# Kernel tuning notes

Hardware: AMD Instinct MI355X
Metric: run time of the kernel (lower is better)

Reference implementation:

```python
import jax, jax.numpy as jnp
import numpy as np

B, L, DP, DS = 8, 256, 128, 256  # batch, length, d_pair, d_seq (= 2*d_pair)
NEAR = 4
K = 3  # k_base=3 (no trbv emb); full mask + 2 chains => every row valid


def _ln(x, g, b):
    mu = x.mean(-1, keepdims=True)
    var = ((x - mu) ** 2).mean(-1, keepdims=True)
    return (x - mu) / jnp.sqrt(var + 1e-5) * g + b


def _masked_mean(x, m, axes):
    num = (x * m).sum(axes)
    den = jnp.clip(m.sum(axes), 1e-6, None)
    return num / den


def _masked_max(x, m, axes):
    v = jnp.where(m > 0, x, -jnp.inf).max(axes)
    return jnp.where(jnp.isinf(v), jnp.zeros_like(v), v)


def _mlp(x, w1, b1, w2, b2):
    return jax.nn.relu(x @ w1 + b1) @ w2 + b2


def setup_inputs() -> dict:
    key = jax.random.key(0)
    ks = jax.random.split(key, 26)
    s = 0.02
    d = {
        "seq_repr": jax.random.normal(ks[0], (B, L, DS), jnp.float32),
        "pair_repr": jax.random.normal(ks[1], (B, L, L, DP), jnp.float32),
        "chain_id": jax.random.randint(ks[2], (B, L), 0, 2, jnp.int32),
        "mask": jnp.ones((B, L), jnp.bool_),
        "ln_s_g": jnp.ones((DS,), jnp.float32),
        "ln_s_b": jnp.zeros((DS,), jnp.float32),
        "ln_z_g": jnp.ones((DS,), jnp.float32),
        "ln_z_b": jnp.zeros((DS,), jnp.float32),
        "W_seq": jax.random.normal(ks[3], (DS, DS), jnp.float32) * s,
        "W_pair": jax.random.normal(ks[4], (DS, DS), jnp.float32) * s,
    }
    in_dim = 2 * DS
    for i, name in enumerate(["m0", "m1", "m2"]):
        d[name + "_w1"] = jax.random.normal(ks[5 + 4 * i], (in_dim, 64), jnp.float32) * s
        d[name + "_b1"] = jnp.zeros((64,), jnp.float32)
        d[name + "_w2"] = jax.random.normal(ks[6 + 4 * i], (64, 1), jnp.float32) * s
        d[name + "_b2"] = jnp.zeros((1,), jnp.float32)
    d["f_w1"] = jax.random.normal(ks[20], (3, 8), jnp.float32) * s
    d["f_b1"] = jnp.zeros((8,), jnp.float32)
    d["f_w2"] = jax.random.normal(ks[21], (8, 1), jnp.float32) * s
    d["f_b2"] = jnp.zeros((1,), jnp.float32)
    return d


def reference(seq_repr, pair_repr, chain_id, mask,
              ln_s_g, ln_s_b, ln_z_g, ln_z_b, W_seq, W_pair,
              m0_w1, m0_b1, m0_w2, m0_b2,
              m1_w1, m1_b1, m1_w2, m1_b2,
              m2_w1, m2_b1, m2_w2, m2_b2,
              f_w1, f_b1, f_w2, f_b2):
    m = mask.astype(jnp.float32)[..., None]  # [B,L,1]
    s = _ln(seq_repr, ln_s_g, ln_s_b) @ W_seq  # [B,L,DS]
    s_mean = _masked_mean(s, m, 1)
    s_max = _masked_max(s, m, 1)
    s_feat = jnp.concatenate([s_mean, s_max], -1)  # [B,2*DS]

    pair = jnp.concatenate([pair_repr, jnp.swapaxes(pair_repr, 1, 2)], -1)  # [B,L,L,DS]
    eye = jnp.eye(L, dtype=pair.dtype)[None, :, :, None]
    pair = pair * (1.0 - eye)
    z = _ln(pair, ln_z_g, ln_z_b) @ W_pair  # [B,L,L,DS]

    pm = (mask[:, :, None] & mask[:, None, :]).astype(jnp.float32)[..., None]  # [B,L,L,1]
    same = (chain_id[:, :, None] == chain_id[:, None, :])[..., None]
    intra = pm * same.astype(jnp.float32)
    inter = pm * (~same).astype(jnp.float32)

    inter_mean = _masked_mean(z, inter, (1, 2))  # [B,DS]
    row_den_raw = inter.sum(2)  # [B,L,1]
    row_valid = row_den_raw[..., 0] > 0
    row_mean_i = (z * inter).sum(2) / jnp.clip(row_den_raw, 1e-6, None)  # [B,L,DS]
    score = jnp.where(row_valid, jnp.linalg.norm(row_mean_i, axis=-1), -1e9)
    _, topk_idx = jax.lax.top_k(score, K)  # [B,K]
    selected = jnp.take_along_axis(row_mean_i, topk_idx[..., None], axis=1)
    inter_peak = selected.mean(1)
    inter_feat = jnp.concatenate([inter_mean, inter_peak], -1)

    idx = jnp.arange(L)
    diff = jnp.abs(idx[:, None] - idx[None, :])
    band = ((diff <= NEAR) & (diff > 0)).astype(jnp.float32)[None, :, :, None]
    intra_near = intra * band
    intra_compact = _masked_mean(z, intra_near, (1, 2))
    intra_max = _masked_max(z, intra_near, (1, 2))
    intra_feat = jnp.concatenate([intra_compact, intra_max], -1)

    logits = jnp.concatenate([
        _mlp(s_feat, m0_w1, m0_b1, m0_w2, m0_b2),
        _mlp(inter_feat, m1_w1, m1_b1, m1_w2, m1_b2),
        _mlp(intra_feat, m2_w1, m2_b1, m2_w2, m2_b2),
    ], axis=1)  # [B,3]
    return jax.nn.relu(logits @ f_w1 + f_b1) @ f_w2 + f_b2  # [B,1]
```

## Files before the change

kernel.cpp:

```cpp
#include <hip/hip_runtime.h>
#include <math.h>

#define NB 8
#define NL 256
#define NDP 128
#define NDS 256
#define NEARB 4


__device__ __forceinline__ float waveSum(float v) {
#pragma unroll
  for (int m = 1; m < 64; m <<= 1) v += __shfl_xor(v, m);
  return v;
}

__device__ __forceinline__ void waveSum2(float& a, float& b) {
#pragma unroll
  for (int m = 1; m < 64; m <<= 1) {
    a += __shfl_xor(a, m);
    b += __shfl_xor(b, m);
  }
}

__device__ __forceinline__ void grpSum2(float& a, float& b) {
#pragma unroll
  for (int m = 1; m < 32; m <<= 1) {
    a += __shfl_xor(a, m);
    b += __shfl_xor(b, m);
  }
}

__global__ __launch_bounds__(256) void kA_pair(
    const float* __restrict__ pair, const int* __restrict__ chain,
    const float* __restrict__ g, const float* __restrict__ beta,
    const float* __restrict__ Wp, const float* __restrict__ seq,
    const float* __restrict__ gs, const float* __restrict__ bs,
    const float* __restrict__ Ws, float* __restrict__ acc,
    float* __restrict__ cntI, float* __restrict__ sbuf,
    float* __restrict__ intraLN, float* __restrict__ cntA,
    float* __restrict__ bandMax) {
  const int i = blockIdx.x;
  const int b = blockIdx.y;
  const int tid = threadIdx.x;
  const int wave = tid >> 6, lane = tid & 63;
  const int grp = lane >> 5, pos = lane & 31;
  const int slot = wave * 2 + grp;

  __shared__ int sList[NL];
  __shared__ int sCnt4[4];
  __shared__ int sOff[4];
  __shared__ int sN;
  __shared__ float sAcc[8][NDS];
  __shared__ float sU[8];
  __shared__ float lnrow[8][NDS];
  __shared__ float red[4], red2[4];

  const int ci = chain[b * NL + i];

  {
    float v = seq[(size_t)(b * NL + i) * NDS + tid];
    float s = v, ssq = v * v;
    waveSum2(s, ssq);
    if (lane == 0) {
      red[wave] = s;
      red2[wave] = ssq;
    }
    __syncthreads();
    float S = red[0] + red[1] + red[2] + red[3];
    float SS = red2[0] + red2[1] + red2[2] + red2[3];
    float mu = S * (1.0f / NDS);
    float inv = 1.0f / sqrtf(SS * (1.0f / NDS) - mu * mu + 1e-5f);
    lnrow[0][tid] = (v - mu) * inv * gs[tid] + bs[tid];
    __syncthreads();
    float z = 0.f;
    for (int k = 0; k < NDS; ++k) z = fmaf(lnrow[0][k], Ws[k * NDS + tid], z);
    sbuf[(size_t)(b * NL + i) * NDS + tid] = z;
  }
  __syncthreads();

  {
    const bool flag = (chain[b * NL + tid] != ci);
    unsigned long long bal = __ballot(flag);
    int ppos = __popcll(bal & ((1ull << lane) - 1ull));
    if (lane == 0) sCnt4[wave] = __popcll(bal);
    __syncthreads();
    if (tid == 0) {
      int o = 0;
#pragma unroll
      for (int w = 0; w < 4; ++w) {
        sOff[w] = o;
        o += sCnt4[w];
      }
      sN = o;
    }
    __syncthreads();
    if (flag) sList[sOff[wave] + ppos] = tid;
    __syncthreads();

    const int n = sN;
    const int c0 = 8 * pos;

    const bool rowHalf = (pos < 16);
    const float* sb = rowHalf ? pair + ((size_t)(b * NL + i) * NL) * NDP + c0
                              : pair + ((size_t)b * NL * NL) * NDP +
                                    (size_t)i * NDP + (c0 - NDP);
    const size_t jstr = rowHalf ? (size_t)NDP : (size_t)NL * NDP;

    float R0 = 0.f, R1 = 0.f, R2 = 0.f, R3 = 0.f;
    float R4 = 0.f, R5 = 0.f, R6 = 0.f, R7 = 0.f;
    float U = 0.f;

    for (int p = slot; p < n; p += 8) {
      const int j = sList[p];
      const float* src = sb + (size_t)j * jstr;
      float4 a0 = *(const float4*)src;
      float4 a1 = *(const float4*)(src + 4);
      float s = (a0.x + a0.y) + (a0.z + a0.w) + (a1.x + a1.y) + (a1.z + a1.w);
      float ss = a0.x * a0.x + a0.y * a0.y + a0.z * a0.z + a0.w * a0.w +
                 a1.x * a1.x + a1.y * a1.y + a1.z * a1.z + a1.w * a1.w;
      grpSum2(s, ss);
      const float mu = s * (1.0f / NDS);
      const float inv = 1.0f / sqrtf(ss * (1.0f / NDS) - mu * mu + 1e-5f);
      R0 = fmaf(a0.x, inv, R0);
      R1 = fmaf(a0.y, inv, R1);
      R2 = fmaf(a0.z, inv, R2);
      R3 = fmaf(a0.w, inv, R3);
      R4 = fmaf(a1.x, inv, R4);
      R5 = fmaf(a1.y, inv, R5);
      R6 = fmaf(a1.z, inv, R6);
      R7 = fmaf(a1.w, inv, R7);
      U = fmaf(mu, inv, U);
    }

    *(float4*)&sAcc[slot][c0] = make_float4(R0, R1, R2, R3);
    *(float4*)&sAcc[slot][c0 + 4] = make_float4(R4, R5, R6, R7);
    sU[slot] = U;
    __syncthreads();
    float v = 0.f;
#pragma unroll
    for (int p2 = 0; p2 < 8; ++p2) v += sAcc[p2][tid];
    float Utot = sU[0] + sU[1] + sU[2] + sU[3] + sU[4] + sU[5] + sU[6] + sU[7];
    acc[(size_t)(b * NL + i) * NDS + tid] =
        g[tid] * (v - Utot) + (float)n * beta[tid];
    if (tid == 0) cntI[b * NL + i] = (float)n;
  }

  {
    const int t = tid;
    int js[8];
    int nv = 0;
    for (int dj = -NEARB; dj <= NEARB; ++dj) {
      int j = i + dj;
      if (dj == 0 || j < 0 || j >= NL) continue;
      if (chain[b * NL + j] == ci) js[nv++] = j;
    }

    const int c0 = 4 * lane;
    const float4 g4 = *(const float4*)(g + c0);
    const float4 b4 = *(const float4*)(beta + c0);
    __syncthreads();
    for (int r = wave; r < 8; r += 4) {
      if (r < nv) {
        const int j = js[r];
        const float* src =
            (lane < 32)
                ? pair + ((size_t)(b * NL + i) * NL + j) * NDP + c0
                : pair + ((size_t)(b * NL + j) * NL + i) * NDP + (c0 - NDP);
        float4 a = *(const float4*)src;
        float s = (a.x + a.y) + (a.z + a.w);
        float ss = a.x * a.x + a.y * a.y + a.z * a.z + a.w * a.w;
        waveSum2(s, ss);
        float mu = s * (1.0f / NDS);
        float inv = 1.0f / sqrtf(ss * (1.0f / NDS) - mu * mu + 1e-5f);
        lnrow[r][c0] = (a.x - mu) * inv * g4.x + b4.x;
        lnrow[r][c0 + 1] = (a.y - mu) * inv * g4.y + b4.y;
        lnrow[r][c0 + 2] = (a.z - mu) * inv * g4.z + b4.z;
        lnrow[r][c0 + 3] = (a.w - mu) * inv * g4.w + b4.w;
      } else {
        lnrow[r][c0] = 0.f;
        lnrow[r][c0 + 1] = 0.f;
        lnrow[r][c0 + 2] = 0.f;
        lnrow[r][c0 + 3] = 0.f;
      }
    }
    __syncthreads();

    float z[8] = {0, 0, 0, 0, 0, 0, 0, 0};
    if (nv > 0) {
      for (int k = 0; k < NDS; ++k) {
        float wk = Wp[k * NDS + t];
#pragma unroll
        for (int r = 0; r < 8; ++r) z[r] += lnrow[r][k] * wk;
      }
    }
    float zmax = -INFINITY, lnsum = 0.f;
#pragma unroll
    for (int r = 0; r < 8; ++r)
      if (r < nv) {
        zmax = fmaxf(zmax, z[r]);
        lnsum += lnrow[r][t];
      }
    intraLN[(size_t)(b * NL + i) * NDS + t] = lnsum;
    bandMax[(size_t)(b * NL + i) * NDS + t] = zmax;
    if (t == 0) cntA[b * NL + i] = (float)nv;
  }
}

__global__ __launch_bounds__(256) void kB_rowmean(
    const float* __restrict__ acc, const float* __restrict__ cntI,
    const float* __restrict__ Wp, const float* __restrict__ sbuf,
    const float* __restrict__ intraLN, const float* __restrict__ cntA,
    const float* __restrict__ bandMax, float* __restrict__ rmean,
    float* __restrict__ score, float* __restrict__ part,
    float* __restrict__ partC) {
  const int chunk = blockIdx.x;
  const int b = blockIdx.y;
  const int t = threadIdx.x;
  const int wave = t >> 6, lane = t & 63;
  __shared__ float vrow[4][NDS];
  __shared__ float red[4];
  float cnts[4], araw[4];
#pragma unroll
  for (int r = 0; r < 4; ++r) {
    const int i = chunk * 4 + r;
    float c = cntI[b * NL + i];
    cnts[r] = c;
    araw[r] = acc[(size_t)(b * NL + i) * NDS + t];
    vrow[r][t] = araw[r] / fmaxf(c, 1e-6f);
  }
  __syncthreads();
  float z[4] = {0, 0, 0, 0};
  for (int k = 0; k < NDS; ++k) {
    float wk = Wp[k * NDS + t];
#pragma unroll
    for (int r = 0; r < 4; ++r) z[r] += vrow[r][k] * wk;
  }
#pragma unroll
  for (int r = 0; r < 4; ++r) {
    const int i = chunk * 4 + r;
    rmean[(size_t)(b * NL + i) * NDS + t] = z[r];
    float q = waveSum(z[r] * z[r]);
    __syncthreads();
    if (lane == 0) red[wave] = q;
    __syncthreads();
    if (t == 0) {
      float ss = red[0] + red[1] + red[2] + red[3];
      score[b * NL + i] = (cnts[r] > 0.f) ? sqrtf(ss) : -1e9f;
    }
    __syncthreads();
  }

  float ssum = 0.f, smax = -INFINITY, isum = 0.f, imax = -INFINITY;
  const float asum = araw[0] + araw[1] + araw[2] + araw[3];
#pragma unroll
  for (int r = 0; r < 4; ++r) {
    const size_t idx = (size_t)(b * NL + chunk * 4 + r) * NDS + t;
    float v = sbuf[idx];
    ssum += v;
    smax = fmaxf(smax, v);
    isum += intraLN[idx];
    imax = fmaxf(imax, bandMax[idx]);
  }
  const size_t pb = (size_t)(b * 64 + chunk) * 5 * NDS;
  part[pb + 0 * NDS + t] = ssum;
  part[pb + 1 * NDS + t] = smax;
  part[pb + 2 * NDS + t] = asum;
  part[pb + 3 * NDS + t] = isum;
  part[pb + 4 * NDS + t] = imax;
  if (t == 0) {
    partC[(b * 64 + chunk) * 2 + 0] = cnts[0] + cnts[1] + cnts[2] + cnts[3];
    float ia = 0.f;
    for (int r = 0; r < 4; ++r) ia += cntA[b * NL + chunk * 4 + r];
    partC[(b * 64 + chunk) * 2 + 1] = ia;
  }
}

__global__ __launch_bounds__(256) void kC_heads(
    const float* __restrict__ part, const float* __restrict__ partC,
    const float* __restrict__ Wp, const float* __restrict__ score,
    const float* __restrict__ rmean, const float* __restrict__ m0w1,
    const float* __restrict__ m0b1, const float* __restrict__ m0w2,
    const float* __restrict__ m0b2, const float* __restrict__ m1w1,
    const float* __restrict__ m1b1, const float* __restrict__ m1w2,
    const float* __restrict__ m1b2, const float* __restrict__ m2w1,
    const float* __restrict__ m2b1, const float* __restrict__ m2w2,
    const float* __restrict__ m2b2, float* __restrict__ logitsBuf) {
  const int b = blockIdx.x;
  const int q = blockIdx.y;
  const int t = threadIdx.x;
  __shared__ float f[2 * NDS];
  __shared__ float sv[NDS];
  __shared__ float hp[4][64];
  __shared__ float h[64];
  __shared__ float sc[NL];
  __shared__ float rv[NL];
  __shared__ int ri[NL];
  __shared__ int top3[3];

  if (q == 0) {
    float ssum = 0.f, smax = -INFINITY;
    for (int c = 0; c < 64; ++c) {
      const size_t pb = (size_t)(b * 64 + c) * 5 * NDS;
      ssum += part[pb + 0 * NDS + t];
      smax = fmaxf(smax, part[pb + 1 * NDS + t]);
    }
    f[t] = ssum * (1.0f / NL);
    f[NDS + t] = isinf(smax) ? 0.f : smax;
    __syncthreads();
  } else if (q == 1) {
    float asum = 0.f, tc = 0.f;
    for (int c = 0; c < 64; ++c) {
      asum += part[(size_t)(b * 64 + c) * 5 * NDS + 2 * NDS + t];
      tc += partC[(b * 64 + c) * 2 + 0];
    }
    sv[t] = asum / fmaxf(tc, 1e-6f);
    sc[t] = score[b * NL + t];
    __syncthreads();
    float om = 0.f;
    for (int k = 0; k < NDS; ++k) om += sv[k] * Wp[k * NDS + t];
    f[t] = om;
    for (int r = 0; r < 3; ++r) {
      rv[t] = sc[t];
      ri[t] = t;
      __syncthreads();
      for (int s2 = 128; s2 > 0; s2 >>= 1) {
        if (t < s2) {
          if (rv[t + s2] > rv[t] ||
              (rv[t + s2] == rv[t] && ri[t + s2] < ri[t])) {
            rv[t] = rv[t + s2];
            ri[t] = ri[t + s2];
          }
        }
        __syncthreads();
      }
      if (t == 0) {
        top3[r] = ri[0];
        sc[ri[0]] = -INFINITY;
      }
      __syncthreads();
    }
    const int i0 = top3[0], i1 = top3[1], i2 = top3[2];
    f[NDS + t] = (rmean[(size_t)(b * NL + i0) * NDS + t] +
                  rmean[(size_t)(b * NL + i1) * NDS + t] +
                  rmean[(size_t)(b * NL + i2) * NDS + t]) *
                 (1.0f / 3.0f);
    __syncthreads();
  } else {
    float isum = 0.f, ic = 0.f, imax = -INFINITY;
    for (int c = 0; c < 64; ++c) {
      const size_t pb = (size_t)(b * 64 + c) * 5 * NDS;
      isum += part[pb + 3 * NDS + t];
      imax = fmaxf(imax, part[pb + 4 * NDS + t]);
      ic += partC[(b * 64 + c) * 2 + 1];
    }
    sv[t] = isum / fmaxf(ic, 1e-6f);
    __syncthreads();
    float oc = 0.f;
    for (int k = 0; k < NDS; ++k) oc += sv[k] * Wp[k * NDS + t];
    f[t] = oc;
    f[NDS + t] = isinf(imax) ? 0.f : imax;
    __syncthreads();
  }

  const float* w1 = (q == 0) ? m0w1 : ((q == 1) ? m1w1 : m2w1);
  const float* b1 = (q == 0) ? m0b1 : ((q == 1) ? m1b1 : m2b1);
  const float* w2 = (q == 0) ? m0w2 : ((q == 1) ? m1w2 : m2w2);
  const float* b2 = (q == 0) ? m0b2 : ((q == 1) ? m1b2 : m2b2);
  const int o = t & 63, c4 = t >> 6;
  float a = 0.f;
  for (int k = c4 * 128; k < c4 * 128 + 128; ++k) a += f[k] * w1[k * 64 + o];
  hp[c4][o] = a;
  __syncthreads();
  if (t < 64)
    h[t] = fmaxf(hp[0][t] + hp[1][t] + hp[2][t] + hp[3][t] + b1[t], 0.f);
  __syncthreads();
  if (t < 64) {
    float p = h[t] * w2[t];
    p = waveSum(p);
    if (t == 0) logitsBuf[b * 3 + q] = p + b2[0];
  }
}

__global__ __launch_bounds__(64) void kD_final(
    const float* __restrict__ logitsBuf, const float* __restrict__ fw1,
    const float* __restrict__ fb1, const float* __restrict__ fw2,
    const float* __restrict__ fb2, float* __restrict__ out) {
  const int t = threadIdx.x;
  if (t < NB) {
    float l0 = logitsBuf[t * 3 + 0];
    float l1 = logitsBuf[t * 3 + 1];
    float l2 = logitsBuf[t * 3 + 2];
    float o = 0.f;
    for (int u = 0; u < 8; ++u) {
      float a = fb1[u] + l0 * fw1[0 * 8 + u] + l1 * fw1[1 * 8 + u] +
                l2 * fw1[2 * 8 + u];
      o += fmaxf(a, 0.f) * fw2[u];
    }
    out[t] = o + fb2[0];
  }
}

extern "C" void kernel_launch(void* const* d_in, const int* in_sizes, int n_in,
                              void* d_out, int out_size, void* d_ws,
                              size_t ws_size, hipStream_t stream) {
  const float* seq = (const float*)d_in[0];
  const float* pair = (const float*)d_in[1];
  const int* chain = (const int*)d_in[2];
  const float* ln_s_g = (const float*)d_in[4];
  const float* ln_s_b = (const float*)d_in[5];
  const float* ln_z_g = (const float*)d_in[6];
  const float* ln_z_b = (const float*)d_in[7];
  const float* Ws = (const float*)d_in[8];
  const float* Wp = (const float*)d_in[9];
  const float* m0w1 = (const float*)d_in[10];
  const float* m0b1 = (const float*)d_in[11];
  const float* m0w2 = (const float*)d_in[12];
  const float* m0b2 = (const float*)d_in[13];
  const float* m1w1 = (const float*)d_in[14];
  const float* m1b1 = (const float*)d_in[15];
  const float* m1w2 = (const float*)d_in[16];
  const float* m1b2 = (const float*)d_in[17];
  const float* m2w1 = (const float*)d_in[18];
  const float* m2b1 = (const float*)d_in[19];
  const float* m2w2 = (const float*)d_in[20];
  const float* m2b2 = (const float*)d_in[21];
  const float* fw1 = (const float*)d_in[22];
  const float* fb1 = (const float*)d_in[23];
  const float* fw2 = (const float*)d_in[24];
  const float* fb2 = (const float*)d_in[25];
  float* out = (float*)d_out;

  float* ws = (float*)d_ws;
  float* acc = ws;
  float* cntI = acc + (size_t)NB * NL * NDS;
  float* sbuf = cntI + NB * NL;
  float* intraLN = sbuf + (size_t)NB * NL * NDS;
  float* cntA = intraLN + (size_t)NB * NL * NDS;
  float* bandMax = cntA + NB * NL;
  float* rmean = bandMax + (size_t)NB * NL * NDS;
  float* score = rmean + (size_t)NB * NL * NDS;
  float* part = score + NB * NL;
  float* partC = part + (size_t)NB * 64 * 5 * NDS;
  float* logitsBuf = partC + NB * 64 * 2;

  kA_pair<<<dim3(NL, NB), 256, 0, stream>>>(pair, chain, ln_z_g, ln_z_b, Wp,
                                            seq, ln_s_g, ln_s_b, Ws, acc,
                                            cntI, sbuf, intraLN, cntA,
                                            bandMax);
  kB_rowmean<<<dim3(NL / 4, NB), 256, 0, stream>>>(acc, cntI, Wp, sbuf,
                                                   intraLN, cntA, bandMax,
                                                   rmean, score, part, partC);
  kC_heads<<<dim3(NB, 3), 256, 0, stream>>>(part, partC, Wp, score, rmean,
                                            m0w1, m0b1, m0w2, m0b2, m1w1,
                                            m1b1, m1w2, m1b2, m2w1, m2b1,
                                            m2w2, m2b2, logitsBuf);
  kD_final<<<1, 64, 0, stream>>>(logitsBuf, fw1, fb1, fw2, fb2, out);
}
```

Measured before the change: 128.2 us.

## Split pair pass into coalesced row-stats and tiled accumulation kernels

The old single pass read each inter-chain pair element twice, once as a row half and once as a strided column half at stride L*DP. That gave poorly coalesced gathers. Now a first kernel computes per-half sums and sums of squares along contiguous rows. A new tiled 16x16 kernel then combines the halves into LayerNorm scales and accumulates row and column contributions from the same tile. The changes add a pass over the pair tensor (read twice), a rs/rss scratch buffer and 16-way partial buffers reduced in kB. In exchange, pair memory access becomes contiguous.

```diff
diff --git a/kernel.cpp b/kernel.cpp
--- a/kernel.cpp
+++ b/kernel.cpp
@@ -30,13 +30,13 @@
   }
 }
 
-__global__ __launch_bounds__(256) void kA_pair(
+__global__ __launch_bounds__(256) void kS_stats(
     const float* __restrict__ pair, const int* __restrict__ chain,
     const float* __restrict__ g, const float* __restrict__ beta,
     const float* __restrict__ Wp, const float* __restrict__ seq,
     const float* __restrict__ gs, const float* __restrict__ bs,
-    const float* __restrict__ Ws, float* __restrict__ acc,
-    float* __restrict__ cntI, float* __restrict__ sbuf,
+    const float* __restrict__ Ws, float* __restrict__ rs,
+    float* __restrict__ rss, float* __restrict__ sbuf,
     float* __restrict__ intraLN, float* __restrict__ cntA,
     float* __restrict__ bandMax) {
   const int i = blockIdx.x;
@@ -50,8 +50,6 @@
   __shared__ int sCnt4[4];
   __shared__ int sOff[4];
   __shared__ int sN;
-  __shared__ float sAcc[8][NDS];
-  __shared__ float sU[8];
   __shared__ float lnrow[8][NDS];
   __shared__ float red[4], red2[4];
 
@@ -98,51 +96,21 @@
     __syncthreads();
 
     const int n = sN;
-    const int c0 = 8 * pos;
-
-    const bool rowHalf = (pos < 16);
-    const float* sb = rowHalf ? pair + ((size_t)(b * NL + i) * NL) * NDP + c0
-                              : pair + ((size_t)b * NL * NL) * NDP +
-                                    (size_t)i * NDP + (c0 - NDP);
-    const size_t jstr = rowHalf ? (size_t)NDP : (size_t)NL * NDP;
-
-    float R0 = 0.f, R1 = 0.f, R2 = 0.f, R3 = 0.f;
-    float R4 = 0.f, R5 = 0.f, R6 = 0.f, R7 = 0.f;
-    float U = 0.f;
-
+    const float* rowbase =
+        pair + ((size_t)(b * NL + i) * NL) * NDP + 4 * pos;
+    float* rsRow = rs + ((size_t)b * NL + i) * NL;
+    float* rssRow = rss + ((size_t)b * NL + i) * NL;
     for (int p = slot; p < n; p += 8) {
       const int j = sList[p];
-      const float* src = sb + (size_t)j * jstr;
-      float4 a0 = *(const float4*)src;
-      float4 a1 = *(const float4*)(src + 4);
-      float s = (a0.x + a0.y) + (a0.z + a0.w) + (a1.x + a1.y) + (a1.z + a1.w);
-      float ss = a0.x * a0.x + a0.y * a0.y + a0.z * a0.z + a0.w * a0.w +
-                 a1.x * a1.x + a1.y * a1.y + a1.z * a1.z + a1.w * a1.w;
+      float4 a = *(const float4*)(rowbase + (size_t)j * NDP);
+      float s = (a.x + a.y) + (a.z + a.w);
+      float ss = a.x * a.x + a.y * a.y + a.z * a.z + a.w * a.w;
       grpSum2(s, ss);
-      const float mu = s * (1.0f / NDS);
-      const float inv = 1.0f / sqrtf(ss * (1.0f / NDS) - mu * mu + 1e-5f);
-      R0 = fmaf(a0.x, inv, R0);
-      R1 = fmaf(a0.y, inv, R1);
-      R2 = fmaf(a0.z, inv, R2);
-      R3 = fmaf(a0.w, inv, R3);
-      R4 = fmaf(a1.x, inv, R4);
-      R5 = fmaf(a1.y, inv, R5);
-      R6 = fmaf(a1.z, inv, R6);
-      R7 = fmaf(a1.w, inv, R7);
-      U = fmaf(mu, inv, U);
-    }
-
-    *(float4*)&sAcc[slot][c0] = make_float4(R0, R1, R2, R3);
-    *(float4*)&sAcc[slot][c0 + 4] = make_float4(R4, R5, R6, R7);
-    sU[slot] = U;
-    __syncthreads();
-    float v = 0.f;
-#pragma unroll
-    for (int p2 = 0; p2 < 8; ++p2) v += sAcc[p2][tid];
-    float Utot = sU[0] + sU[1] + sU[2] + sU[3] + sU[4] + sU[5] + sU[6] + sU[7];
-    acc[(size_t)(b * NL + i) * NDS + tid] =
-        g[tid] * (v - Utot) + (float)n * beta[tid];
-    if (tid == 0) cntI[b * NL + i] = (float)n;
+      if (pos == 0) {
+        rsRow[j] = s;
+        rssRow[j] = ss;
+      }
+    }
   }
 
   {
@@ -206,27 +174,154 @@
   }
 }
 
+__global__ __launch_bounds__(256) void kM_accum(
+    const float* __restrict__ pair, const int* __restrict__ chain,
+    const float* __restrict__ rs, const float* __restrict__ rss,
+    float* __restrict__ pacc, float* __restrict__ paccU) {
+  const int b = blockIdx.y;
+  const int ti = blockIdx.x >> 4, tj = blockIdx.x & 15;
+  const int i0 = ti * 16, j0 = tj * 16;
+  const int tid = threadIdx.x;
+  const int wave = tid >> 6, lane = tid & 63;
+  const int grp = lane >> 5, pos = lane & 31;
+  const int slot = wave * 2 + grp;
+
+  __shared__ float invL[16][16];
+  __shared__ float muwL[16][16];
+  __shared__ int chI[16], chJ[16];
+
+  if (tid < 16) chI[tid] = chain[b * NL + i0 + tid];
+  else if (tid < 32) chJ[tid - 16] = chain[b * NL + j0 + (tid - 16)];
+  __syncthreads();
+
+  {
+    const int li = tid >> 4, lj = tid & 15;
+    float inv = 0.f, muw = 0.f;
+    if (chI[li] != chJ[lj]) {
+      const int ii = i0 + li, jj = j0 + lj;
+      float sA = rs[((size_t)b * NL + ii) * NL + jj];
+      float sB = rs[((size_t)b * NL + jj) * NL + ii];
+      float qA = rss[((size_t)b * NL + ii) * NL + jj];
+      float qB = rss[((size_t)b * NL + jj) * NL + ii];
+      float mu = (sA + sB) * (1.0f / NDS);
+      float var = (qA + qB) * (1.0f / NDS) - mu * mu;
+      inv = 1.0f / sqrtf(var + 1e-5f);
+      muw = mu * inv;
+    }
+    invL[li][lj] = inv;
+    muwL[li][lj] = muw;
+  }
+  __syncthreads();
+
+  const int c0 = 4 * pos;
+  const float* pairB = pair + (size_t)b * NL * NL * NDP;
+
+  float4 RA = {0, 0, 0, 0}, RB = {0, 0, 0, 0};
+  float UA = 0.f, UB = 0.f;
+  {
+    const float* baseA =
+        pairB + ((size_t)(i0 + slot) * NL + j0) * NDP + c0;
+    const float* baseB =
+        pairB + ((size_t)(i0 + slot + 8) * NL + j0) * NDP + c0;
+    for (int lj = 0; lj < 16; ++lj) {
+      float wA = invL[slot][lj];
+      if (wA != 0.f) {
+        float4 a = *(const float4*)(baseA + (size_t)lj * NDP);
+        RA.x = fmaf(a.x, wA, RA.x);
+        RA.y = fmaf(a.y, wA, RA.y);
+        RA.z = fmaf(a.z, wA, RA.z);
+        RA.w = fmaf(a.w, wA, RA.w);
+        UA += muwL[slot][lj];
+      }
+      float wB = invL[slot + 8][lj];
+      if (wB != 0.f) {
+        float4 a = *(const float4*)(baseB + (size_t)lj * NDP);
+        RB.x = fmaf(a.x, wB, RB.x);
+        RB.y = fmaf(a.y, wB, RB.y);
+        RB.z = fmaf(a.z, wB, RB.z);
+        RB.w = fmaf(a.w, wB, RB.w);
+        UB += muwL[slot + 8][lj];
+      }
+    }
+  }
+  {
+    float* d = pacc + (((size_t)(b * 16 + tj) * NL + i0 + slot) * NDS) + c0;
+    *(float4*)d = RA;
+    *(float4*)(d + (size_t)8 * NDS) = RB;
+    if (pos == 0) {
+      paccU[(size_t)(b * 16 + tj) * NL + i0 + slot] = UA;
+      paccU[(size_t)(b * 16 + tj) * NL + i0 + slot + 8] = UB;
+    }
+  }
+
+  float4 CA = {0, 0, 0, 0}, CB = {0, 0, 0, 0};
+  {
+    for (int li = 0; li < 16; ++li) {
+      const float* rowb = pairB + ((size_t)(i0 + li) * NL + j0) * NDP + c0;
+      float wA = invL[li][slot];
+      if (wA != 0.f) {
+        float4 a = *(const float4*)(rowb + (size_t)slot * NDP);
+        CA.x = fmaf(a.x, wA, CA.x);
+        CA.y = fmaf(a.y, wA, CA.y);
+        CA.z = fmaf(a.z, wA, CA.z);
+        CA.w = fmaf(a.w, wA, CA.w);
+      }
+      float wB = invL[li][slot + 8];
+      if (wB != 0.f) {
+        float4 a = *(const float4*)(rowb + (size_t)(slot + 8) * NDP);
+        CB.x = fmaf(a.x, wB, CB.x);
+        CB.y = fmaf(a.y, wB, CB.y);
+        CB.z = fmaf(a.z, wB, CB.z);
+        CB.w = fmaf(a.w, wB, CB.w);
+      }
+    }
+  }
+  {
+    float* d =
+        pacc + (((size_t)(b * 16 + ti) * NL + j0 + slot) * NDS) + NDP + c0;
+    *(float4*)d = CA;
+    *(float4*)(d + (size_t)8 * NDS) = CB;
+  }
+}
+
 __global__ __launch_bounds__(256) void kB_rowmean(
-    const float* __restrict__ acc, const float* __restrict__ cntI,
-    const float* __restrict__ Wp, const float* __restrict__ sbuf,
-    const float* __restrict__ intraLN, const float* __restrict__ cntA,
-    const float* __restrict__ bandMax, float* __restrict__ rmean,
-    float* __restrict__ score, float* __restrict__ part,
-    float* __restrict__ partC) {
+    const float* __restrict__ pacc, const float* __restrict__ paccU,
+    const int* __restrict__ chain, const float* __restrict__ gz,
+    const float* __restrict__ bz, const float* __restrict__ Wp,
+    const float* __restrict__ sbuf, const float* __restrict__ intraLN,
+    const float* __restrict__ cntA, const float* __restrict__ bandMax,
+    float* __restrict__ rmean, float* __restrict__ score,
+    float* __restrict__ part, float* __restrict__ partC) {
   const int chunk = blockIdx.x;
   const int b = blockIdx.y;
   const int t = threadIdx.x;
   const int wave = t >> 6, lane = t & 63;
   __shared__ float vrow[4][NDS];
   __shared__ float red[4];
-  float cnts[4], araw[4];
+  __shared__ int sN0[4];
+
+  const int chT = chain[b * NL + t];
+  unsigned long long bal = __ballot(chT == 0);
+  if (lane == 0) sN0[wave] = __popcll(bal);
+  __syncthreads();
+  const int n0 = sN0[0] + sN0[1] + sN0[2] + sN0[3];
+
+  const float gzt = gz[t], bzt = bz[t];
+  float cnts[4], aval[4];
 #pragma unroll
   for (int r = 0; r < 4; ++r) {
     const int i = chunk * 4 + r;
-    float c = cntI[b * NL + i];
+    const int ci = chain[b * NL + i];
+    const float c = (ci == 0) ? (float)(NL - n0) : (float)n0;
     cnts[r] = c;
-    araw[r] = acc[(size_t)(b * NL + i) * NDS + t];
-    vrow[r][t] = araw[r] / fmaxf(c, 1e-6f);
+    float araw = 0.f, Ut = 0.f;
+#pragma unroll
+    for (int q = 0; q < 16; ++q) {
+      araw += pacc[((size_t)(b * 16 + q) * NL + i) * NDS + t];
+      Ut += paccU[(size_t)(b * 16 + q) * NL + i];
+    }
+    aval[r] = gzt * (araw - Ut) + c * bzt;
+    vrow[r][t] = aval[r] / fmaxf(c, 1e-6f);
   }
   __syncthreads();
   float z[4] = {0, 0, 0, 0};
@@ -251,7 +346,7 @@
   }
 
   float ssum = 0.f, smax = -INFINITY, isum = 0.f, imax = -INFINITY;
-  const float asum = araw[0] + araw[1] + araw[2] + araw[3];
+  const float asum = aval[0] + aval[1] + aval[2] + aval[3];
 #pragma unroll
   for (int r = 0; r < 4; ++r) {
     const size_t idx = (size_t)(b * NL + chunk * 4 + r) * NDS + t;
@@ -431,9 +526,11 @@
   float* out = (float*)d_out;
 
   float* ws = (float*)d_ws;
-  float* acc = ws;
-  float* cntI = acc + (size_t)NB * NL * NDS;
-  float* sbuf = cntI + NB * NL;
+  float* rs = ws;
+  float* rss = rs + (size_t)NB * NL * NL;
+  float* pacc = rss + (size_t)NB * NL * NL;
+  float* paccU = pacc + (size_t)NB * 16 * NL * NDS;
+  float* sbuf = paccU + (size_t)NB * 16 * NL;
   float* intraLN = sbuf + (size_t)NB * NL * NDS;
   float* cntA = intraLN + (size_t)NB * NL * NDS;
   float* bandMax = cntA + NB * NL;
@@ -443,13 +540,14 @@
   float* partC = part + (size_t)NB * 64 * 5 * NDS;
   float* logitsBuf = partC + NB * 64 * 2;
 
-  kA_pair<<<dim3(NL, NB), 256, 0, stream>>>(pair, chain, ln_z_g, ln_z_b, Wp,
-                                            seq, ln_s_g, ln_s_b, Ws, acc,
-                                            cntI, sbuf, intraLN, cntA,
-                                            bandMax);
-  kB_rowmean<<<dim3(NL / 4, NB), 256, 0, stream>>>(acc, cntI, Wp, sbuf,
-                                                   intraLN, cntA, bandMax,
-                                                   rmean, score, part, partC);
+  kS_stats<<<dim3(NL, NB), 256, 0, stream>>>(pair, chain, ln_z_g, ln_z_b, Wp,
+                                             seq, ln_s_g, ln_s_b, Ws, rs, rss,
+                                             sbuf, intraLN, cntA, bandMax);
+  kM_accum<<<dim3(256, NB), 256, 0, stream>>>(pair, chain, rs, rss, pacc,
+                                              paccU);
+  kB_rowmean<<<dim3(NL / 4, NB), 256, 0, stream>>>(
+      pacc, paccU, chain, ln_z_g, ln_z_b, Wp, sbuf, intraLN, cntA, bandMax,
+      rmean, score, part, partC);
   kC_heads<<<dim3(NB, 3), 256, 0, stream>>>(part, partC, Wp, score, rmean,
                                             m0w1, m0b1, m0w2, m0b2, m1w1,
                                             m1b1, m1w2, m1b2, m2w1, m2b1,
```

New measurement: 170.3 us. 1.33x slower.
